# Performance work log

Hardware: AMD Instinct MI355X
Metric: run time of the kernel (lower is better)

The kernel has to match this reference:

```python
import jax, jax.numpy as jnp
import numpy as np

B, N, D, P, V = 8, 256, 300, 128, 50001  # batch, seq len, emb dim, proj dim, vocab(+unk)


def setup_inputs() -> dict:
    key = jax.random.key(0)
    ks = jax.random.split(key, 10)
    s = 1.0 / np.sqrt(D)
    sp = 1.0 / np.sqrt(P)
    emb = jax.random.normal(ks[0], (V, D), jnp.float32)
    emb = emb.at[-1].set(0.0)  # unk row zeroed, matches add_unk
    return {
        "sentence": jax.random.randint(ks[1], (B, N), 0, V),
        "emb": emb,
        "Wl": jax.random.uniform(ks[2], (P, D), jnp.float32, -s, s),
        "bl": jnp.zeros((P,), jnp.float32),
        "Wr": jax.random.uniform(ks[3], (P, D), jnp.float32, -s, s),
        "Wo": jax.random.uniform(ks[4], (1, P), jnp.float32, -sp, sp),
        "bo": jnp.zeros((1,), jnp.float32),
        "Ws1": jax.random.uniform(ks[5], (P, D), jnp.float32, -s, s),
        "bs1": jnp.zeros((P,), jnp.float32),
        "Ws2": jax.random.uniform(ks[6], (1, P), jnp.float32, -sp, sp),
        "bs2": jnp.zeros((1,), jnp.float32),
        "We1": jax.random.uniform(ks[7], (P, D), jnp.float32, -s, s),
        "be1": jnp.zeros((P,), jnp.float32),
        "We2": jax.random.uniform(ks[8], (1, P), jnp.float32, -sp, sp),
        "be2": jnp.zeros((1,), jnp.float32),
    }


def reference(sentence, emb, Wl, bl, Wr, Wo, bo, Ws1, bs1, Ws2, bs2, We1, be1, We2, be2):
    x = emb[sentence]                                   # [B,N,D] embedding lookup
    start = jax.nn.relu(x @ Ws1.T + bs1) @ Ws2.T + bs2  # [B,N,1]
    end = jax.nn.relu(x @ We1.T + be1) @ We2.T + be2    # [B,N,1]
    left = x @ Wl.T + bl                                # [B,N,P]
    right = x @ Wr.T                                    # [B,N,P]
    # proj[b,i,j,p] = left[b,j,p] + right[b,i,p]  (unsqueeze(1) + unsqueeze(2))
    proj = left[:, None, :, :] + right[:, :, None, :]   # [B,N,N,P]
    bigram = jax.nn.relu(proj) @ Wo.T + bo              # [B,N,N,1]
    return (bigram, start, end)
```

## Files before the change

kernel.cpp:

```cpp
#include <hip/hip_runtime.h>

#define NB 8
#define NN 256
#define DD 300
#define PP 128
#define NC 512
#define OFF_S (NB * NN * NN)
#define OFF_E (NB * NN * NN + NB * NN)

typedef unsigned short u16;
typedef unsigned int   u32;

__device__ __forceinline__ float bf2f(u16 u) {
    union { u32 i; float f; } v;
    v.i = ((u32)u) << 16;
    return v.f;
}
__device__ __forceinline__ u16 f2bf(float f) {
    union { float f; u32 i; } v;
    v.f = f;
    u32 lsb = (v.i >> 16) & 1u;
    v.i += 0x7fffu + lsb;
    return (u16)(v.i >> 16);
}

template<bool BF>
__device__ __forceinline__ float4 ld4(const void* base, int idx) {
    if (BF) {
        ushort4 e = *(const ushort4*)((const u16*)base + idx);
        return make_float4(bf2f(e.x), bf2f(e.y), bf2f(e.z), bf2f(e.w));
    } else {
        return *(const float4*)((const float*)base + idx);
    }
}
template<bool BF>
__device__ __forceinline__ float ld1(const void* base, int idx) {
    return BF ? bf2f(((const u16*)base)[idx]) : ((const float*)base)[idx];
}
template<bool BF>
__device__ __forceinline__ void st1(void* base, int idx, float v) {
    if (BF) ((u16*)base)[idx] = f2bf(v);
    else    ((float*)base)[idx] = v;
}
template<bool BF>
__device__ __forceinline__ void st4(void* base, int idx, float4 v) {
    if (BF) {
        ushort4 o = make_ushort4(f2bf(v.x), f2bf(v.y), f2bf(v.z), f2bf(v.w));
        *(ushort4*)((u16*)base + idx) = o;
    } else {
        *(float4*)((float*)base + idx) = v;
    }
}
__device__ __forceinline__ float4 rfma4(float4 l, float r, float w, float4 a) {
    a.x = fmaf(fmaxf(l.x + r, 0.f), w, a.x);
    a.y = fmaf(fmaxf(l.y + r, 0.f), w, a.y);
    a.z = fmaf(fmaxf(l.z + r, 0.f), w, a.z);
    a.w = fmaf(fmaxf(l.w + r, 0.f), w, a.w);
    return a;
}

extern "C" __global__ void detect_kernel(const u32* __restrict__ embU,
                                         int* __restrict__ flag) {
    int lane = threadIdx.x;
    int cnt = 0;
    for (int i = lane; i < 256; i += 64) {
        u32 w = embU[i];
        union { u32 u; float f; } v;
        v.u = (w & 0xFFFFu) << 16;
        float a = fabsf(v.f);
        if (a == 0.f || (a >= 0.00390625f && a <= 256.f)) cnt++;
    }
    #pragma unroll
    for (int off = 32; off; off >>= 1) cnt += __shfl_down(cnt, off, 64);
    if (lane == 0) *flag = (cnt >= 128) ? 1 : 0;
}

template<bool BF>
__device__ __forceinline__ void prep_body(
    const void* __restrict__ Wl, const void* __restrict__ Wr,
    const void* __restrict__ Ws1, const void* __restrict__ We1,
    float* __restrict__ WTf, float (*tile)[301])
{
    const int tid = threadIdx.x;
    const int c0  = blockIdx.x * 32;

    for (int e = tid; e < 32 * 75; e += 256) {
        int r = e / 75;
        int q = e - r * 75;
        int c = c0 + r;
        const void* src = (c < 128) ? Wl : (c < 256) ? Wr
                        : (c < 384) ? Ws1 : We1;
        float4 f = ld4<BF>(src, (c & 127) * DD + 4 * q);
        tile[r][4 * q + 0] = f.x;
        tile[r][4 * q + 1] = f.y;
        tile[r][4 * q + 2] = f.z;
        tile[r][4 * q + 3] = f.w;
    }
    __syncthreads();
    for (int e = tid; e < 300 * 32; e += 256) {
        int k = e >> 5;
        int c = e & 31;
        WTf[(size_t)k * NC + c0 + c] = tile[c][k];
    }
}

extern "C" __global__ void __launch_bounds__(256)
prep_kernel(const void* __restrict__ Wl, const void* __restrict__ Wr,
            const void* __restrict__ Ws1, const void* __restrict__ We1,
            float* __restrict__ WTf, const int* __restrict__ flag)
{
    __shared__ float tile[32][301];
    if (*flag) prep_body<true >(Wl, Wr, Ws1, We1, WTf, tile);
    else       prep_body<false>(Wl, Wr, Ws1, We1, WTf, tile);
}

template<bool BF>
__device__ __forceinline__ void tok_body(
    const int* __restrict__ sent, const void* __restrict__ emb,
    const float* __restrict__ WTf,
    const void* __restrict__ bl,
    const void* __restrict__ bs1, const void* __restrict__ Ws2,
    const void* __restrict__ bs2,
    const void* __restrict__ be1, const void* __restrict__ We2,
    const void* __restrict__ be2,
    float* __restrict__ leftT, float* __restrict__ rightW,
    void* __restrict__ out, float (*sxT)[4], int* sids)
{
    const int tid = threadIdx.x;
    const int t0  = blockIdx.x * 4;

    if (tid < 4) sids[tid] = sent[t0 + tid];
    __syncthreads();

    for (int e = tid; e < DD * 4; e += 256) {
        int k = e >> 2, t = e & 3;
        sxT[k][t] = ld1<BF>(emb, sids[t] * DD + k);
    }
    __syncthreads();

    float a0[4], a1[4];
    #pragma unroll
    for (int t = 0; t < 4; ++t) { a0[t] = 0.f; a1[t] = 0.f; }

    const float* wp = WTf + 2 * tid;
    #pragma unroll 4
    for (int k = 0; k < DD; ++k) {
        float2 w  = *(const float2*)(wp + (size_t)k * NC);
        float4 xa = *(const float4*)&sxT[k][0];
        a0[0] = fmaf(xa.x, w.x, a0[0]); a1[0] = fmaf(xa.x, w.y, a1[0]);
        a0[1] = fmaf(xa.y, w.x, a0[1]); a1[1] = fmaf(xa.y, w.y, a1[1]);
        a0[2] = fmaf(xa.z, w.x, a0[2]); a1[2] = fmaf(xa.z, w.y, a1[2]);
        a0[3] = fmaf(xa.w, w.x, a0[3]); a1[3] = fmaf(xa.w, w.y, a1[3]);
    }

    const int wv = tid >> 6;
    const int l  = tid & 63;
    const int p0 = 2 * l, p1 = p0 + 1;

    if (wv == 0) {
        float b0 = ld1<BF>(bl, p0), b1 = ld1<BF>(bl, p1);
        #pragma unroll
        for (int t = 0; t < 4; ++t) {
            int tg = t0 + t, bb = tg >> 8, jj = tg & 255;
            leftT[((size_t)bb * PP + p0) * NN + jj] = a0[t] + b0;
            leftT[((size_t)bb * PP + p1) * NN + jj] = a1[t] + b1;
        }
    } else if (wv == 1) {
        #pragma unroll
        for (int t = 0; t < 4; ++t) {
            rightW[(size_t)(t0 + t) * PP + p0] = a0[t];
            rightW[(size_t)(t0 + t) * PP + p1] = a1[t];
        }
    } else {
        const void* h1 = (wv == 2) ? bs1 : be1;
        const void* h2 = (wv == 2) ? Ws2 : We2;
        const void* h3 = (wv == 2) ? bs2 : be2;
        float b0 = ld1<BF>(h1, p0), b1 = ld1<BF>(h1, p1);
        float w0 = ld1<BF>(h2, p0), w1 = ld1<BF>(h2, p1);
        float v[4];
        #pragma unroll
        for (int t = 0; t < 4; ++t)
            v[t] = fmaxf(a0[t] + b0, 0.f) * w0 + fmaxf(a1[t] + b1, 0.f) * w1;
        #pragma unroll
        for (int off = 32; off; off >>= 1) {
            #pragma unroll
            for (int t = 0; t < 4; ++t) v[t] += __shfl_down(v[t], off, 64);
        }
        if (l == 0) {
            float b2 = ld1<BF>(h3, 0);
            int base = (wv == 2) ? OFF_S : OFF_E;
            #pragma unroll
            for (int t = 0; t < 4; ++t)
                st1<BF>(out, base + t0 + t, v[t] + b2);
        }
    }
}

extern "C" __global__ void __launch_bounds__(256)
tok_kernel(const int* __restrict__ sent, const void* __restrict__ emb,
           const float* __restrict__ WTf,
           const void* __restrict__ bl,
           const void* __restrict__ bs1, const void* __restrict__ Ws2,
           const void* __restrict__ bs2,
           const void* __restrict__ be1, const void* __restrict__ We2,
           const void* __restrict__ be2,
           float* __restrict__ leftT, float* __restrict__ rightW,
           void* __restrict__ out, const int* __restrict__ flag)
{
    __shared__ __align__(16) float sxT[DD][4];
    __shared__ int sids[4];
    if (*flag) {
        tok_body<true >(sent, emb, WTf, bl, bs1, Ws2, bs2, be1, We2, be2,
                        leftT, rightW, out, sxT, sids);
    } else {
        tok_body<false>(sent, emb, WTf, bl, bs1, Ws2, bs2, be1, We2, be2,
                        leftT, rightW, out, sxT, sids);
    }
}

template<bool BF>
__device__ __forceinline__ void big_body(
    const float* __restrict__ leftT, const float* __restrict__ rightW,
    const void* __restrict__ Wo, const void* __restrict__ bo,
    void* __restrict__ outB,
    float (*sR)[128], float* sWo, float4 (*red4)[64][4])
{
    const int tid = threadIdx.x;
    const int b   = blockIdx.x >> 6;
    const int i0  = (blockIdx.x & 63) << 2;

    if (tid < 128) sWo[tid] = ld1<BF>(Wo, tid);
    for (int c = tid; c < 512; c += 256) {
        int i = c >> 7, pp = c & 127;
        sR[i][pp] = rightW[((size_t)(b * NN + i0 + i)) * PP + pp];
    }
    __syncthreads();

    const int w    = tid >> 6;
    const int lane = tid & 63;
    const int j4   = lane << 2;
    const float* lp = leftT + (size_t)b * PP * NN + j4;

    float4 A0 = {0.f, 0.f, 0.f, 0.f}, A1 = A0, A2 = A0, A3 = A0;
    const int pbase = w * 32;
    #pragma unroll
    for (int g = 0; g < 8; ++g) {
        const int p = pbase + g * 4;
        float4 wo = *(const float4*)&sWo[p];
        float4 r0 = *(const float4*)&sR[0][p];
        float4 r1 = *(const float4*)&sR[1][p];
        float4 r2 = *(const float4*)&sR[2][p];
        float4 r3 = *(const float4*)&sR[3][p];
        const float* lpp = lp + (size_t)p * NN;
        float4 l0 = *(const float4*)(lpp);
        float4 l1 = *(const float4*)(lpp + NN);
        float4 l2 = *(const float4*)(lpp + 2 * NN);
        float4 l3 = *(const float4*)(lpp + 3 * NN);
        A0 = rfma4(l0, r0.x, wo.x, A0);
        A1 = rfma4(l0, r1.x, wo.x, A1);
        A2 = rfma4(l0, r2.x, wo.x, A2);
        A3 = rfma4(l0, r3.x, wo.x, A3);
        A0 = rfma4(l1, r0.y, wo.y, A0);
        A1 = rfma4(l1, r1.y, wo.y, A1);
        A2 = rfma4(l1, r2.y, wo.y, A2);
        A3 = rfma4(l1, r3.y, wo.y, A3);
        A0 = rfma4(l2, r0.z, wo.z, A0);
        A1 = rfma4(l2, r1.z, wo.z, A1);
        A2 = rfma4(l2, r2.z, wo.z, A2);
        A3 = rfma4(l2, r3.z, wo.z, A3);
        A0 = rfma4(l3, r0.w, wo.w, A0);
        A1 = rfma4(l3, r1.w, wo.w, A1);
        A2 = rfma4(l3, r2.w, wo.w, A2);
        A3 = rfma4(l3, r3.w, wo.w, A3);
    }

    red4[w][lane][0] = A0;
    red4[w][lane][1] = A1;
    red4[w][lane][2] = A2;
    red4[w][lane][3] = A3;
    __syncthreads();

    if (tid < 64) {
        float bov = ld1<BF>(bo, 0);
        #pragma unroll
        for (int i = 0; i < 4; ++i) {
            float4 s0 = red4[0][tid][i];
            float4 s1 = red4[1][tid][i];
            float4 s2 = red4[2][tid][i];
            float4 s3 = red4[3][tid][i];
            float4 s;
            s.x = s0.x + s1.x + s2.x + s3.x + bov;
            s.y = s0.y + s1.y + s2.y + s3.y + bov;
            s.z = s0.z + s1.z + s2.z + s3.z + bov;
            s.w = s0.w + s1.w + s2.w + s3.w + bov;
            st4<BF>(outB, (int)(((size_t)(b * NN + i0 + i)) * NN) + tid * 4, s);
        }
    }
}

extern "C" __global__ void __launch_bounds__(256)
big_kernel(const float* __restrict__ leftT, const float* __restrict__ rightW,
           const void* __restrict__ Wo, const void* __restrict__ bo,
           void* __restrict__ outB, const int* __restrict__ flag)
{
    __shared__ float sR[4][128];
    __shared__ float sWo[128];
    __shared__ float4 red4[4][64][4];
    if (*flag) big_body<true >(leftT, rightW, Wo, bo, outB, sR, sWo, red4);
    else       big_body<false>(leftT, rightW, Wo, bo, outB, sR, sWo, red4);
}

extern "C" void kernel_launch(void* const* d_in, const int* in_sizes, int n_in,
                              void* d_out, int out_size, void* d_ws, size_t ws_size,
                              hipStream_t stream) {
    const int*  sent = (const int*)d_in[0];
    const void* emb  = d_in[1];
    const void* Wl   = d_in[2];
    const void* bl   = d_in[3];
    const void* Wr   = d_in[4];
    const void* Wo   = d_in[5];
    const void* bo   = d_in[6];
    const void* Ws1  = d_in[7];
    const void* bs1  = d_in[8];
    const void* Ws2  = d_in[9];
    const void* bs2  = d_in[10];
    const void* We1  = d_in[11];
    const void* be1  = d_in[12];
    const void* We2  = d_in[13];
    const void* be2  = d_in[14];

    int*   flag   = (int*)d_ws;
    float* leftT  = (float*)((char*)d_ws + 1024);
    float* rightW = leftT + (size_t)NB * PP * NN;
    float* WTf    = rightW + (size_t)NB * NN * PP;

    hipLaunchKernelGGL(detect_kernel, dim3(1), dim3(64), 0, stream,
                       (const u32*)emb, flag);
    hipLaunchKernelGGL(prep_kernel, dim3(16), dim3(256), 0, stream,
                       Wl, Wr, Ws1, We1, WTf, flag);
    hipLaunchKernelGGL(tok_kernel, dim3(512), dim3(256), 0, stream,
                       sent, emb, WTf, bl, bs1, Ws2, bs2, be1, We2, be2,
                       leftT, rightW, d_out, flag);
    hipLaunchKernelGGL(big_kernel, dim3(512), dim3(256), 0, stream,
                       leftT, rightW, Wo, bo, d_out, flag);
}
```

Baseline: 159.5 us.

## Fold dtype detection into kernels and double tokens per tok block

Removes the separate single-wave detect kernel by having one wave in each block recompute the dtype flag and broadcast it through shared memory, which saves a launch and a serial dependency. The token kernel now handles 8 tokens per block instead of 4, halving the grid, so each weight load from WTf is reused across twice as many tokens. Weight loads are software-pipelined six rows ahead. In exchange, every block repeats the small flag scan, register pressure rises from 16 accumulators, and tok_body reloads sids redundantly.

```diff
diff --git a/kernel.cpp b/kernel.cpp
--- a/kernel.cpp
+++ b/kernel.cpp
@@ -59,9 +59,8 @@
     return a;
 }
 
-extern "C" __global__ void detect_kernel(const u32* __restrict__ embU,
-                                         int* __restrict__ flag) {
-    int lane = threadIdx.x;
+__device__ __forceinline__ int flag_wave(const u32* __restrict__ embU) {
+    int lane = threadIdx.x & 63;
     int cnt = 0;
     for (int i = lane; i < 256; i += 64) {
         u32 w = embU[i];
@@ -71,8 +70,8 @@
         if (a == 0.f || (a >= 0.00390625f && a <= 256.f)) cnt++;
     }
     #pragma unroll
-    for (int off = 32; off; off >>= 1) cnt += __shfl_down(cnt, off, 64);
-    if (lane == 0) *flag = (cnt >= 128) ? 1 : 0;
+    for (int off = 32; off; off >>= 1) cnt += __shfl_xor(cnt, off, 64);
+    return (cnt >= 128) ? 1 : 0;
 }
 
 template<bool BF>
@@ -107,10 +106,16 @@
 extern "C" __global__ void __launch_bounds__(256)
 prep_kernel(const void* __restrict__ Wl, const void* __restrict__ Wr,
             const void* __restrict__ Ws1, const void* __restrict__ We1,
-            float* __restrict__ WTf, const int* __restrict__ flag)
+            float* __restrict__ WTf, const u32* __restrict__ embU)
 {
     __shared__ float tile[32][301];
-    if (*flag) prep_body<true >(Wl, Wr, Ws1, We1, WTf, tile);
+    __shared__ int sflag;
+    if (threadIdx.x < 64) {
+        int f = flag_wave(embU);
+        if (threadIdx.x == 0) sflag = f;
+    }
+    __syncthreads();
+    if (sflag) prep_body<true >(Wl, Wr, Ws1, We1, WTf, tile);
     else       prep_body<false>(Wl, Wr, Ws1, We1, WTf, tile);
 }
 
@@ -124,34 +129,53 @@
     const void* __restrict__ be1, const void* __restrict__ We2,
     const void* __restrict__ be2,
     float* __restrict__ leftT, float* __restrict__ rightW,
-    void* __restrict__ out, float (*sxT)[4], int* sids)
+    void* __restrict__ out, float (*sxT)[8], int* sids)
 {
     const int tid = threadIdx.x;
-    const int t0  = blockIdx.x * 4;
-
-    if (tid < 4) sids[tid] = sent[t0 + tid];
-    __syncthreads();
-
-    for (int e = tid; e < DD * 4; e += 256) {
-        int k = e >> 2, t = e & 3;
+    const int t0  = blockIdx.x * 8;
+
+    if (tid < 8) sids[tid] = sent[t0 + tid];
+    __syncthreads();
+
+    for (int e = tid; e < DD * 8; e += 256) {
+        int k = e >> 3, t = e & 7;
         sxT[k][t] = ld1<BF>(emb, sids[t] * DD + k);
     }
     __syncthreads();
 
-    float a0[4], a1[4];
+    float a0[8], a1[8];
     #pragma unroll
-    for (int t = 0; t < 4; ++t) { a0[t] = 0.f; a1[t] = 0.f; }
+    for (int t = 0; t < 8; ++t) { a0[t] = 0.f; a1[t] = 0.f; }
 
     const float* wp = WTf + 2 * tid;
-    #pragma unroll 4
-    for (int k = 0; k < DD; ++k) {
-        float2 w  = *(const float2*)(wp + (size_t)k * NC);
-        float4 xa = *(const float4*)&sxT[k][0];
-        a0[0] = fmaf(xa.x, w.x, a0[0]); a1[0] = fmaf(xa.x, w.y, a1[0]);
-        a0[1] = fmaf(xa.y, w.x, a0[1]); a1[1] = fmaf(xa.y, w.y, a1[1]);
-        a0[2] = fmaf(xa.z, w.x, a0[2]); a1[2] = fmaf(xa.z, w.y, a1[2]);
-        a0[3] = fmaf(xa.w, w.x, a0[3]); a1[3] = fmaf(xa.w, w.y, a1[3]);
-    }
+#define LW(kk) (*(const float2*)(wp + (size_t)(kk) * NC))
+#define FMAK(kk, Wv) do {                                               \
+        float4 xa = *(const float4*)&sxT[(kk)][0];                      \
+        float4 xb = *(const float4*)&sxT[(kk)][4];                      \
+        float wx_ = (Wv).x, wy_ = (Wv).y;                               \
+        a0[0]=fmaf(xa.x,wx_,a0[0]); a1[0]=fmaf(xa.x,wy_,a1[0]);         \
+        a0[1]=fmaf(xa.y,wx_,a0[1]); a1[1]=fmaf(xa.y,wy_,a1[1]);         \
+        a0[2]=fmaf(xa.z,wx_,a0[2]); a1[2]=fmaf(xa.z,wy_,a1[2]);         \
+        a0[3]=fmaf(xa.w,wx_,a0[3]); a1[3]=fmaf(xa.w,wy_,a1[3]);         \
+        a0[4]=fmaf(xb.x,wx_,a0[4]); a1[4]=fmaf(xb.x,wy_,a1[4]);         \
+        a0[5]=fmaf(xb.y,wx_,a0[5]); a1[5]=fmaf(xb.y,wy_,a1[5]);         \
+        a0[6]=fmaf(xb.z,wx_,a0[6]); a1[6]=fmaf(xb.z,wy_,a1[6]);         \
+        a0[7]=fmaf(xb.w,wx_,a0[7]); a1[7]=fmaf(xb.w,wy_,a1[7]);         \
+    } while (0)
+
+    float2 q0 = LW(0), q1 = LW(1), q2 = LW(2),
+           q3 = LW(3), q4 = LW(4), q5 = LW(5);
+    for (int k = 0; k < DD; k += 6) {
+        float2 u0 = q0, u1 = q1, u2 = q2, u3 = q3, u4 = q4, u5 = q5;
+        if (k + 6 < DD) {
+            q0 = LW(k + 6);  q1 = LW(k + 7);  q2 = LW(k + 8);
+            q3 = LW(k + 9);  q4 = LW(k + 10); q5 = LW(k + 11);
+        }
+        FMAK(k + 0, u0); FMAK(k + 1, u1); FMAK(k + 2, u2);
+        FMAK(k + 3, u3); FMAK(k + 4, u4); FMAK(k + 5, u5);
+    }
+#undef LW
+#undef FMAK
 
     const int wv = tid >> 6;
     const int l  = tid & 63;
@@ -159,15 +183,14 @@
 
     if (wv == 0) {
         float b0 = ld1<BF>(bl, p0), b1 = ld1<BF>(bl, p1);
-        #pragma unroll
-        for (int t = 0; t < 4; ++t) {
-            int tg = t0 + t, bb = tg >> 8, jj = tg & 255;
-            leftT[((size_t)bb * PP + p0) * NN + jj] = a0[t] + b0;
-            leftT[((size_t)bb * PP + p1) * NN + jj] = a1[t] + b1;
-        }
+        const int bb = t0 >> 8, j0 = t0 & 255;
+        float* o0 = leftT + ((size_t)bb * PP + p0) * NN + j0;
+        float* o1 = leftT + ((size_t)bb * PP + p1) * NN + j0;
+        #pragma unroll
+        for (int t = 0; t < 8; ++t) { o0[t] = a0[t] + b0; o1[t] = a1[t] + b1; }
     } else if (wv == 1) {
         #pragma unroll
-        for (int t = 0; t < 4; ++t) {
+        for (int t = 0; t < 8; ++t) {
             rightW[(size_t)(t0 + t) * PP + p0] = a0[t];
             rightW[(size_t)(t0 + t) * PP + p1] = a1[t];
         }
@@ -176,21 +199,21 @@
         const void* h2 = (wv == 2) ? Ws2 : We2;
         const void* h3 = (wv == 2) ? bs2 : be2;
         float b0 = ld1<BF>(h1, p0), b1 = ld1<BF>(h1, p1);
-        float w0 = ld1<BF>(h2, p0), w1 = ld1<BF>(h2, p1);
-        float v[4];
-        #pragma unroll
-        for (int t = 0; t < 4; ++t)
-            v[t] = fmaxf(a0[t] + b0, 0.f) * w0 + fmaxf(a1[t] + b1, 0.f) * w1;
+        float w0h = ld1<BF>(h2, p0), w1h = ld1<BF>(h2, p1);
+        float v[8];
+        #pragma unroll
+        for (int t = 0; t < 8; ++t)
+            v[t] = fmaxf(a0[t] + b0, 0.f) * w0h + fmaxf(a1[t] + b1, 0.f) * w1h;
         #pragma unroll
         for (int off = 32; off; off >>= 1) {
             #pragma unroll
-            for (int t = 0; t < 4; ++t) v[t] += __shfl_down(v[t], off, 64);
+            for (int t = 0; t < 8; ++t) v[t] += __shfl_down(v[t], off, 64);
         }
         if (l == 0) {
             float b2 = ld1<BF>(h3, 0);
             int base = (wv == 2) ? OFF_S : OFF_E;
             #pragma unroll
-            for (int t = 0; t < 4; ++t)
+            for (int t = 0; t < 8; ++t)
                 st1<BF>(out, base + t0 + t, v[t] + b2);
         }
     }
@@ -205,11 +228,18 @@
            const void* __restrict__ be1, const void* __restrict__ We2,
            const void* __restrict__ be2,
            float* __restrict__ leftT, float* __restrict__ rightW,
-           void* __restrict__ out, const int* __restrict__ flag)
-{
-    __shared__ __align__(16) float sxT[DD][4];
-    __shared__ int sids[4];
-    if (*flag) {
+           void* __restrict__ out)
+{
+    __shared__ __align__(16) float sxT[DD][8];
+    __shared__ int sids[8];
+    __shared__ int sflag;
+    if (threadIdx.x < 64) {
+        int f = flag_wave((const u32*)emb);
+        if (threadIdx.x == 0) sflag = f;
+    }
+    if (threadIdx.x < 8) sids[threadIdx.x] = sent[blockIdx.x * 8 + threadIdx.x];
+    __syncthreads();
+    if (sflag) {
         tok_body<true >(sent, emb, WTf, bl, bs1, Ws2, bs2, be1, We2, be2,
                         leftT, rightW, out, sxT, sids);
     } else {
@@ -301,12 +331,18 @@
 extern "C" __global__ void __launch_bounds__(256)
 big_kernel(const float* __restrict__ leftT, const float* __restrict__ rightW,
            const void* __restrict__ Wo, const void* __restrict__ bo,
-           void* __restrict__ outB, const int* __restrict__ flag)
+           void* __restrict__ outB, const u32* __restrict__ embU)
 {
     __shared__ float sR[4][128];
     __shared__ float sWo[128];
     __shared__ float4 red4[4][64][4];
-    if (*flag) big_body<true >(leftT, rightW, Wo, bo, outB, sR, sWo, red4);
+    __shared__ int sflag;
+    if (threadIdx.x < 64) {
+        int f = flag_wave(embU);
+        if (threadIdx.x == 0) sflag = f;
+    }
+    __syncthreads();
+    if (sflag) big_body<true >(leftT, rightW, Wo, bo, outB, sR, sWo, red4);
     else       big_body<false>(leftT, rightW, Wo, bo, outB, sR, sWo, red4);
 }
 
@@ -329,18 +365,15 @@
     const void* We2  = d_in[13];
     const void* be2  = d_in[14];
 
-    int*   flag   = (int*)d_ws;
     float* leftT  = (float*)((char*)d_ws + 1024);
     float* rightW = leftT + (size_t)NB * PP * NN;
     float* WTf    = rightW + (size_t)NB * NN * PP;
 
-    hipLaunchKernelGGL(detect_kernel, dim3(1), dim3(64), 0, stream,
-                       (const u32*)emb, flag);
     hipLaunchKernelGGL(prep_kernel, dim3(16), dim3(256), 0, stream,
-                       Wl, Wr, Ws1, We1, WTf, flag);
-    hipLaunchKernelGGL(tok_kernel, dim3(512), dim3(256), 0, stream,
+                       Wl, Wr, Ws1, We1, WTf, (const u32*)emb);
+    hipLaunchKernelGGL(tok_kernel, dim3(256), dim3(256), 0, stream,
                        sent, emb, WTf, bl, bs1, Ws2, bs2, be1, We2, be2,
-                       leftT, rightW, d_out, flag);
+                       leftT, rightW, d_out);
     hipLaunchKernelGGL(big_kernel, dim3(512), dim3(256), 0, stream,
-                       leftT, rightW, Wo, bo, d_out, flag);
-}
+                       leftT, rightW, Wo, bo, d_out, (const u32*)emb);
+}
```

Measured after the change: 155.2 us. 2.7% less time.
